# Kernel optimization log

Hardware: AMD Instinct MI355X
Metric: run time of the kernel (lower is better)

The kernel has to match this reference:

```python
import jax, jax.numpy as jnp
import numpy as np

B, T, D_IN, D_OUT, H = 128, 128, 64, 64, 1024


def _lstm_cell(x_t, h, c, W_ih, W_hh, b_ih, b_hh):
    # PyTorch LSTMCell: gates = x@W_ih^T + b_ih + h@W_hh^T + b_hh, order [i, f, g, o]
    g = x_t @ W_ih.T + b_ih + h @ W_hh.T + b_hh  # [B, 4H]
    i, f, gg, o = jnp.split(g, 4, axis=-1)
    c_new = jax.nn.sigmoid(f) * c + jax.nn.sigmoid(i) * jnp.tanh(gg)
    h_new = jax.nn.sigmoid(o) * jnp.tanh(c_new)
    return h_new, c_new


def setup_inputs() -> dict:
    key = jax.random.key(0)
    ks = jax.random.split(key, 16)
    s_in = 1.0 / np.sqrt(H)
    inp = {
        "x": jax.random.normal(ks[0], (B, T, D_IN), dtype=jnp.float32),
        "W_ih1": jax.random.normal(ks[1], (4 * H, D_IN), dtype=jnp.float32) * s_in,
        "W_hh1": jax.random.normal(ks[2], (4 * H, H), dtype=jnp.float32) * s_in,
        "b_ih1": jax.random.normal(ks[3], (4 * H,), dtype=jnp.float32) * s_in,
        "b_hh1": jax.random.normal(ks[4], (4 * H,), dtype=jnp.float32) * s_in,
        "W_ih2": jax.random.normal(ks[5], (4 * H, H), dtype=jnp.float32) * s_in,
        "W_hh2": jax.random.normal(ks[6], (4 * H, H), dtype=jnp.float32) * s_in,
        "b_ih2": jax.random.normal(ks[7], (4 * H,), dtype=jnp.float32) * s_in,
        "b_hh2": jax.random.normal(ks[8], (4 * H,), dtype=jnp.float32) * s_in,
        "W_lin": jax.random.normal(ks[9], (D_IN, H), dtype=jnp.float32) * s_in,
        "b_lin": jax.random.normal(ks[10], (D_IN,), dtype=jnp.float32) * s_in,
        "W_hio": jax.random.normal(ks[11], (D_OUT, H), dtype=jnp.float32) * s_in,
        "b_hio": jax.random.normal(ks[12], (D_OUT,), dtype=jnp.float32) * s_in,
        "future": 1,
    }
    return inp


def reference(x, W_ih1, W_hh1, b_ih1, b_hh1, W_ih2, W_hh2, b_ih2, b_hh2,
              W_lin, b_lin, W_hio, b_hio, future):
    b = x.shape[0]
    h1 = jnp.zeros((b, H), x.dtype)
    c1 = jnp.zeros((b, H), x.dtype)
    h2 = jnp.zeros((b, H), x.dtype)
    c2 = jnp.zeros((b, H), x.dtype)

    def step(carry, x_t):
        h1, c1, h2, c2 = carry
        h1, c1 = _lstm_cell(x_t, h1, c1, W_ih1, W_hh1, b_ih1, b_hh1)
        h2, c2 = _lstm_cell(h1, h2, c2, W_ih2, W_hh2, b_ih2, b_hh2)
        return (h1, c1, h2, c2), None

    (h1, c1, h2, c2), _ = jax.lax.scan(step, (h1, c1, h2, c2),
                                       jnp.swapaxes(x, 0, 1))  # scan over T
    output = h2 @ W_lin.T + b_lin  # [B, D_IN] (only last step's value is used)

    for _ in range(int(future)):
        h1, c1 = _lstm_cell(output, h1, c1, W_ih1, W_hh1, b_ih1, b_hh1)
        h2, c2 = _lstm_cell(h1, h2, c2, W_ih2, W_hh2, b_ih2, b_hh2)
        output = h2 @ W_hio.T + b_hio  # [B, D_OUT]

    return output[:, None, :]  # [B, 1, D_OUT]
```

## Files before the change

kernel.cpp:

```cpp
#include <hip/hip_runtime.h>

#define B_   128
#define T_   128
#define DIN  64
#define H_   1024
#define NBLK 256
#define NTHR 1024

typedef _Float16 f16;
typedef _Float16 half8 __attribute__((ext_vector_type(8)));
typedef float float4v __attribute__((ext_vector_type(4)));
typedef unsigned uint2v __attribute__((ext_vector_type(2)));
typedef unsigned uint4v __attribute__((ext_vector_type(4)));


#define OFF_W2    34816
#define OFF_SG1A  100352
#define OFF_SG1B  109056
#define OFF_SG2A  117760
#define OFF_SG2B  126464
#define OFF_C1    135168
#define OFF_C2    137216
#define OFF_B1    139264
#define OFF_B2    139328
#define SMEM_BYTES 139392


struct Params {
  const float *x, *Wih1, *Whh1, *bih1, *bhh1, *Wih2, *Whh2, *bih2, *bhh2,
              *Wlin, *blin, *Whio, *bhio;
  const int* fut;
  float* out;
  f16 *x16, *h1a, *h1b, *h2a, *h2b, *ob;
  unsigned *arrive, *rel;
  unsigned *S;
};

__device__ __forceinline__ float sigm(float v) { return 1.f / (1.f + __expf(-v)); }
__device__ __forceinline__ float tanh_(float v) { return 2.f / (1.f + __expf(-2.f * v)) - 1.f; }

__device__ __forceinline__ unsigned get_xcc() {
  unsigned x;
  asm volatile("s_getreg_b32 %0, hwreg(HW_REG_XCC_ID)" : "=s"(x));
  return x & 15u;
}

__device__ __forceinline__ void grid_sync(unsigned* arrive, unsigned* rel, unsigned ph) {
  __syncthreads();
  const int tid = threadIdx.x, bid = blockIdx.x;
  if (bid == 0) {
    if (tid > 0 && tid < NBLK) {
      while (__hip_atomic_load(&arrive[tid], __ATOMIC_RELAXED, __HIP_MEMORY_SCOPE_AGENT) != ph)
        __builtin_amdgcn_s_sleep(8);
    }
    __syncthreads();
    if (tid == 0)
      __hip_atomic_store(rel, ph, __ATOMIC_RELEASE, __HIP_MEMORY_SCOPE_AGENT);
  } else {
    if (tid == 0) {
      __hip_atomic_store(&arrive[bid], ph, __ATOMIC_RELEASE, __HIP_MEMORY_SCOPE_AGENT);
      while (__hip_atomic_load(rel, __ATOMIC_RELAXED, __HIP_MEMORY_SCOPE_AGENT) != ph)
        __builtin_amdgcn_s_sleep(8);
    }
  }
  __syncthreads();
  __builtin_amdgcn_fence(__ATOMIC_ACQUIRE, "agent");
}

__device__ __forceinline__ void fast_sync(unsigned* S, unsigned x, unsigned xtotal,
                                          unsigned nxcd, unsigned ph) {
  __syncthreads();
  if (threadIdx.x == 0) {
    unsigned t = __hip_atomic_fetch_add(&S[x * 32], 1u, __ATOMIC_RELAXED, __HIP_MEMORY_SCOPE_AGENT);
    bool leader = (t % xtotal == 0u);
    if ((t + 1u) % xtotal == 0u) {
      unsigned c = __hip_atomic_fetch_add(&S[512], 1u, __ATOMIC_RELAXED, __HIP_MEMORY_SCOPE_AGENT);
      if ((c + 1u) % nxcd == 0u)
        __hip_atomic_store(&S[544], ph, __ATOMIC_RELAXED, __HIP_MEMORY_SCOPE_AGENT);
      asm volatile("buffer_inv sc0 sc1\n\ts_waitcnt vmcnt(0)" ::: "memory");
      __hip_atomic_store(&S[1088 + x * 32], ph, __ATOMIC_RELAXED, __HIP_MEMORY_SCOPE_AGENT);
    }
    if (leader) {
      while (__hip_atomic_load(&S[544], __ATOMIC_RELAXED, __HIP_MEMORY_SCOPE_AGENT) != ph)
        __builtin_amdgcn_s_sleep(1);
      while (__hip_atomic_load(&S[1088 + x * 32], __ATOMIC_RELAXED, __HIP_MEMORY_SCOPE_AGENT) != ph)
        __builtin_amdgcn_s_sleep(1);
      __hip_atomic_store(&S[576 + x * 32], ph, __ATOMIC_RELAXED, __HIP_MEMORY_SCOPE_AGENT);
      asm volatile("buffer_inv sc0\n\ts_waitcnt vmcnt(0)" ::: "memory");
    } else {
      while (__hip_atomic_load(&S[576 + x * 32], __ATOMIC_RELAXED, __HIP_MEMORY_SCOPE_AGENT) != ph)
        __builtin_amdgcn_s_sleep(2);
      asm volatile("buffer_inv sc0\n\ts_waitcnt vmcnt(0)" ::: "memory");
    }
  }
  __syncthreads();
}

__global__ void __launch_bounds__(NTHR, 4) lstm_k(Params p) {
  extern __shared__ char smem[];
  f16*   W1s  = (f16*)(smem);
  f16*   W2s  = (f16*)(smem + OFF_W2);
  float* Sg1A = (float*)(smem + OFF_SG1A);
  float* Sg1B = (float*)(smem + OFF_SG1B);
  float* Sg2A = (float*)(smem + OFF_SG2A);
  float* Sg2B = (float*)(smem + OFF_SG2B);
  float* c1   = (float*)(smem + OFF_C1);
  float* c2   = (float*)(smem + OFF_C2);
  float* bs1  = (float*)(smem + OFF_B1);
  float* bs2  = (float*)(smem + OFF_B2);

  const int tid = threadIdx.x, bid = blockIdx.x;
  const int hb  = bid * 4;
  const int fut = p.fut[0];
  const unsigned xcc = get_xcc();
  unsigned* S = p.S;

  if (bid == 0) {
    for (int i = tid; i < 2048; i += NTHR)
      __hip_atomic_store(&S[i], 0u, __ATOMIC_RELAXED, __HIP_MEMORY_SCOPE_AGENT);
  }

  for (int idx = tid; idx < 34 * 512; idx += NTHR) {
    int c = idx >> 9, r = idx & 511;
    int q = r >> 7, colw = (r >> 3) & 15, j = r & 7;
    int k = c * 32 + q * 8 + j;
    int row = (colw >> 2) * H_ + hb + (colw & 3);
    float v = (k < H_) ? p.Whh1[row * H_ + k] : p.Wih1[row * DIN + (k - H_)];
    W1s[idx] = (f16)v;
  }
  for (int idx = tid; idx < 64 * 512; idx += NTHR) {
    int c = idx >> 9, r = idx & 511;
    int q = r >> 7, colw = (r >> 3) & 15, j = r & 7;
    int k = c * 32 + q * 8 + j;
    int row = (colw >> 2) * H_ + hb + (colw & 3);
    float v = (k < H_) ? p.Wih2[row * H_ + k] : p.Whh2[row * H_ + (k - H_)];
    W2s[idx] = (f16)v;
  }
  if (tid < 16) {
    int row = (tid >> 2) * H_ + hb + (tid & 3);
    bs1[tid] = p.bih1[row] + p.bhh1[row];
    bs2[tid] = p.bih2[row] + p.bhh2[row];
  }
  for (int i = tid; i < 512; i += NTHR) { c1[i] = 0.f; c2[i] = 0.f; }
  for (int i = bid * NTHR + tid; i < B_ * T_ * DIN; i += NBLK * NTHR)
    p.x16[i] = (f16)p.x[i];
  for (int i = bid * NTHR + tid; i < B_ * H_; i += NBLK * NTHR) {
    p.h1a[i] = (f16)0.f; p.h1b[i] = (f16)0.f;
    p.h2a[i] = (f16)0.f; p.h2b[i] = (f16)0.f;
  }

  unsigned ph = 1;
  grid_sync(p.arrive, p.rel, ph);
  if (tid == 0)
    __hip_atomic_fetch_add(&S[1600 + xcc], 1u, __ATOMIC_RELAXED, __HIP_MEMORY_SCOPE_AGENT);
  ++ph;
  grid_sync(p.arrive, p.rel, ph);

  unsigned xtotal = __hip_atomic_load(&S[1600 + xcc], __ATOMIC_RELAXED, __HIP_MEMORY_SCOPE_AGENT);
  unsigned nxcd = 0;
  for (int i = 0; i < 16; ++i)
    nxcd += (__hip_atomic_load(&S[1600 + i], __ATOMIC_RELAXED, __HIP_MEMORY_SCOPE_AGENT) != 0u);

  auto gsync = [&]() { ++ph; fast_sync(S, xcc, xtotal, nxcd, ph); };

  const int lane = tid & 63, wq = tid >> 6;
  const int g  = wq >> 3;
  const int wv = wq & 7;
  const int col = lane & 15, quad = lane >> 4;
  const int m0 = wv * 16 + col;
  const int ko = quad * 8;
  const int jb = g * 16;
  const float b1v = g ? 0.f : bs1[col];
  const float b2v = g ? 0.f : bs2[col];
  const f16* W1f = W1s + lane * 8;
  const f16* W2f = W2s + lane * 8;
  float* S1w = g ? Sg1B : Sg1A;
  float* S2w = g ? Sg2B : Sg2A;
  const int hoff = quad * 1024 + m0 * 4;

  f16 *h1c = p.h1a, *h1n = p.h1b, *h2c = p.h2a, *h2n = p.h2b;

  auto lstm_pw = [&](const float* SgA, const float* SgB, float* cst, f16* hn) {
    int mm = tid >> 2, cc = tid & 3;
    int i0 = mm * 17 + cc;
    float gi = SgA[i0]      + SgB[i0];
    float gf = SgA[i0 + 4]  + SgB[i0 + 4];
    float gg = SgA[i0 + 8]  + SgB[i0 + 8];
    float go = SgA[i0 + 12] + SgB[i0 + 12];
    float cn = sigm(gf) * cst[tid] + sigm(gi) * tanh_(gg);
    cst[tid] = cn;
    f16 hv = (f16)(sigm(go) * tanh_(cn));
    int v = (int)__builtin_bit_cast(unsigned short, hv);
    int base = lane & ~3;
    int v0 = __shfl(v, base, 64),     v1 = __shfl(v, base + 1, 64);
    int v2 = __shfl(v, base + 2, 64), v3 = __shfl(v, base + 3, 64);
    if (cc == 0) {
      unsigned long long pk = (unsigned long long)(unsigned short)v0
        | ((unsigned long long)(unsigned short)v1 << 16)
        | ((unsigned long long)(unsigned short)v2 << 32)
        | ((unsigned long long)(unsigned short)v3 << 48);
      __hip_atomic_store((unsigned long long*)(hn + bid * 512 + mm * 4), pk,
                         __ATOMIC_RELAXED, __HIP_MEMORY_SCOPE_AGENT);
    }
  };

  auto ldwin = [&](const f16* hX, int j) -> half8 {
    const uint2v* q0 = (const uint2v*)(hX + j * 4096 + hoff);
    const uint2v* q1 = (const uint2v*)(hX + j * 4096 + hoff + 512);
    uint2v u0 = *q0, u1 = *q1;
    uint4v u = {u0[0], u0[1], u1[0], u1[1]};
    return __builtin_bit_cast(half8, u);
  };

  auto phase = [&](bool l1, bool l2, const f16* xp, int xstr) {
    float4v a1 = {b1v, b1v, b1v, b1v};
    float4v a2 = {b2v, b2v, b2v, b2v};

    if (l1) {
      half8 ax = *(const half8*)(xp + m0 * xstr + g * 32 + ko);
      a1 = __builtin_amdgcn_mfma_f32_16x16x32_f16(ax, *(const half8*)(W1f + (32 + g) * 512), a1, 0, 0, 0);
    }
    if (l1 && l2) {
      #pragma unroll
      for (int i = 0; i < 16; ++i) {
        int j = jb + i;
        half8 w1 = ldwin(h1c, j);
        half8 w2 = ldwin(h2c, j);
        a1 = __builtin_amdgcn_mfma_f32_16x16x32_f16(w1, *(const half8*)(W1f + j * 512), a1, 0, 0, 0);
        a2 = __builtin_amdgcn_mfma_f32_16x16x32_f16(w1, *(const half8*)(W2f + j * 512), a2, 0, 0, 0);
        a2 = __builtin_amdgcn_mfma_f32_16x16x32_f16(w2, *(const half8*)(W2f + (32 + j) * 512), a2, 0, 0, 0);
      }
    } else if (l1) {
      #pragma unroll
      for (int i = 0; i < 16; ++i) {
        int j = jb + i;
        half8 w1 = ldwin(h1c, j);
        a1 = __builtin_amdgcn_mfma_f32_16x16x32_f16(w1, *(const half8*)(W1f + j * 512), a1, 0, 0, 0);
      }
    } else if (l2) {
      #pragma unroll
      for (int i = 0; i < 16; ++i) {
        int j = jb + i;
        half8 w1 = ldwin(h1c, j);
        half8 w2 = ldwin(h2c, j);
        a2 = __builtin_amdgcn_mfma_f32_16x16x32_f16(w1, *(const half8*)(W2f + j * 512), a2, 0, 0, 0);
        a2 = __builtin_amdgcn_mfma_f32_16x16x32_f16(w2, *(const half8*)(W2f + (32 + j) * 512), a2, 0, 0, 0);
      }
    }

    __syncthreads();
    if (l1) {
      #pragma unroll
      for (int r = 0; r < 4; ++r)
        S1w[(wv * 16 + quad * 4 + r) * 17 + col] = a1[r];
    }
    if (l2) {
      #pragma unroll
      for (int r = 0; r < 4; ++r)
        S2w[(wv * 16 + quad * 4 + r) * 17 + col] = a2[r];
    }
    __syncthreads();
    if (tid < 512) {
      if (l1) lstm_pw(Sg1A, Sg1B, c1, h1n);
      if (l2) lstm_pw(Sg2A, Sg2B, c2, h2n);
    }
  };

  auto out_phase = [&](const float* W, const float* bv, bool wout) {
    if (tid >= 512) return;
    int j = bid & 63, mgp = bid >> 6;
    int rid = tid >> 4, ks = tid & 15;
    int mrow = mgp * 32 + rid;
    const float* wr = W + j * H_ + ks * 64;
    float s = 0.f;
    #pragma unroll
    for (int q = 0; q < 16; ++q) {
      const uint2v* hp = (const uint2v*)(h2c + (ks * 16 + q) * 512 + mrow * 4);
      uint2v u = *hp;
      half8 hv4;
      { uint4v t = {u[0], u[1], 0u, 0u}; hv4 = __builtin_bit_cast(half8, t); }
      s += (float)hv4[0] * wr[q * 4 + 0] + (float)hv4[1] * wr[q * 4 + 1]
         + (float)hv4[2] * wr[q * 4 + 2] + (float)hv4[3] * wr[q * 4 + 3];
    }
    s += __shfl_down(s, 8, 16);
    s += __shfl_down(s, 4, 16);
    s += __shfl_down(s, 2, 16);
    s += __shfl_down(s, 1, 16);
    if (ks == 0) {
      float v = s + bv[j];
      f16 hv = (f16)v;
      __hip_atomic_store((unsigned short*)&p.ob[mrow * 64 + j],
                         __builtin_bit_cast(unsigned short, hv),
                         __ATOMIC_RELAXED, __HIP_MEMORY_SCOPE_AGENT);
      if (wout) p.out[mrow * 64 + j] = v;
    }
  };

  for (int t = -1; t < T_; ++t) {
    bool l1 = (t + 1 < T_), l2 = (t >= 0);
    phase(l1, l2, p.x16 + (t + 1) * DIN, T_ * DIN);
    gsync();
    if (l1) { f16* tm = h1c; h1c = h1n; h1n = tm; }
    if (l2) { f16* tm = h2c; h2c = h2n; h2n = tm; }
  }
  out_phase(p.Wlin, p.blin, fut == 0);
  gsync();
  for (int f = 0; f < fut; ++f) {
    phase(true, false, p.ob, 64);
    gsync();
    { f16* tm = h1c; h1c = h1n; h1n = tm; }
    phase(false, true, p.ob, 64);
    gsync();
    { f16* tm = h2c; h2c = h2n; h2n = tm; }
    out_phase(p.Whio, p.bhio, f == fut - 1);
    gsync();
  }
}

extern "C" void kernel_launch(void* const* d_in, const int* in_sizes, int n_in,
                              void* d_out, int out_size, void* d_ws, size_t ws_size,
                              hipStream_t stream) {
  char* w = (char*)d_ws;
  auto carve = [&](size_t n) { char* r = w; w += (n + 255) & ~(size_t)255; return r; };

  Params p;
  p.x    = (const float*)d_in[0];
  p.Wih1 = (const float*)d_in[1];
  p.Whh1 = (const float*)d_in[2];
  p.bih1 = (const float*)d_in[3];
  p.bhh1 = (const float*)d_in[4];
  p.Wih2 = (const float*)d_in[5];
  p.Whh2 = (const float*)d_in[6];
  p.bih2 = (const float*)d_in[7];
  p.bhh2 = (const float*)d_in[8];
  p.Wlin = (const float*)d_in[9];
  p.blin = (const float*)d_in[10];
  p.Whio = (const float*)d_in[11];
  p.bhio = (const float*)d_in[12];
  p.fut  = (const int*)d_in[13];
  p.out  = (float*)d_out;

  p.x16 = (f16*)carve((size_t)B_ * T_ * DIN * 2);
  p.h1a = (f16*)carve((size_t)B_ * H_ * 2);
  p.h1b = (f16*)carve((size_t)B_ * H_ * 2);
  p.h2a = (f16*)carve((size_t)B_ * H_ * 2);
  p.h2b = (f16*)carve((size_t)B_ * H_ * 2);
  p.ob  = (f16*)carve((size_t)B_ * 64 * 2);
  p.arrive = (unsigned*)carve(NBLK * sizeof(unsigned));
  p.rel    = (unsigned*)carve(256);
  p.S      = (unsigned*)carve(2048 * sizeof(unsigned));

  (void)hipFuncSetAttribute((const void*)lstm_k,
                            hipFuncAttributeMaxDynamicSharedMemorySize, SMEM_BYTES);
  void* args[] = { &p };
  (void)hipLaunchCooperativeKernel((void*)lstm_k, dim3(NBLK), dim3(NTHR),
                                   args, SMEM_BYTES, stream);
}
```

Baseline: 1.897 ms.

## Split hidden-unit pairs across block pairs with split-K partial exchange via global buffers

Each pair of blocks (bid and bid^128) now shares 8 hidden units. Each block computes the half of the K dimension selected by g for both 4-unit groups, then passes the partial sums for its partner's units through a global buffer. A per-block flag with a spin-wait synchronises the two blocks. Within a block, the two wave-groups split K into halves and the layer-1 and layer-2 pointwise updates run on separate thread halves. The goal is to cut the per-block h-window loads, since each block now reads only half of h1/h2, and to spread the pointwise work. The cost is extra global partial-sum traffic and a pairwise handshake every timestep.

After: 1.890 ms. Within noise of the previous version (-0.4%).

```diff
diff --git a/kernel.cpp b/kernel.cpp
--- a/kernel.cpp
+++ b/kernel.cpp
@@ -12,7 +12,6 @@
 typedef float float4v __attribute__((ext_vector_type(4)));
 typedef unsigned uint2v __attribute__((ext_vector_type(2)));
 typedef unsigned uint4v __attribute__((ext_vector_type(4)));
-
 
 #define OFF_W2    34816
 #define OFF_SG1A  100352
@@ -25,7 +24,6 @@
 #define OFF_B2    139328
 #define SMEM_BYTES 139392
 
-
 struct Params {
   const float *x, *Wih1, *Whh1, *bih1, *bhh1, *Wih2, *Whh2, *bih2, *bhh2,
               *Wlin, *blin, *Whio, *bhio;
@@ -34,6 +32,8 @@
   f16 *x16, *h1a, *h1b, *h2a, *h2b, *ob;
   unsigned *arrive, *rel;
   unsigned *S;
+  float* PB;
+  unsigned* FL;
 };
 
 __device__ __forceinline__ float sigm(float v) { return 1.f / (1.f + __expf(-v)); }
@@ -110,7 +110,10 @@
   float* bs2  = (float*)(smem + OFF_B2);
 
   const int tid = threadIdx.x, bid = blockIdx.x;
-  const int hb  = bid * 4;
+  const int c   = bid & 127;
+  const int g   = bid >> 7;
+  const int bidp = bid ^ 128;
+  const int cb  = c * 2 + g;
   const int fut = p.fut[0];
   const unsigned xcc = get_xcc();
   unsigned* S = p.S;
@@ -119,25 +122,31 @@
     for (int i = tid; i < 2048; i += NTHR)
       __hip_atomic_store(&S[i], 0u, __ATOMIC_RELAXED, __HIP_MEMORY_SCOPE_AGENT);
   }
-
-  for (int idx = tid; idx < 34 * 512; idx += NTHR) {
-    int c = idx >> 9, r = idx & 511;
-    int q = r >> 7, colw = (r >> 3) & 15, j = r & 7;
-    int k = c * 32 + q * 8 + j;
-    int row = (colw >> 2) * H_ + hb + (colw & 3);
-    float v = (k < H_) ? p.Whh1[row * H_ + k] : p.Wih1[row * DIN + (k - H_)];
+  for (int i = bid * NTHR + tid; i < 256 * 32; i += NBLK * NTHR)
+    __hip_atomic_store(&p.FL[i], 0u, __ATOMIC_RELAXED, __HIP_MEMORY_SCOPE_AGENT);
+
+  for (int idx = tid; idx < 17 * 2 * 512; idx += NTHR) {
+    int j2 = idx >> 9, r = idx & 511;
+    int j = j2 >> 1, nt = j2 & 1;
+    int lane_ = r >> 3, jj = r & 7;
+    int q = lane_ >> 4, colw = lane_ & 15;
+    int row = (colw >> 2) * H_ + c * 8 + nt * 4 + (colw & 3);
+    float v = (j < 16) ? p.Whh1[row * H_ + g * 512 + j * 32 + q * 8 + jj]
+                       : p.Wih1[row * DIN + g * 32 + q * 8 + jj];
     W1s[idx] = (f16)v;
   }
-  for (int idx = tid; idx < 64 * 512; idx += NTHR) {
-    int c = idx >> 9, r = idx & 511;
-    int q = r >> 7, colw = (r >> 3) & 15, j = r & 7;
-    int k = c * 32 + q * 8 + j;
-    int row = (colw >> 2) * H_ + hb + (colw & 3);
-    float v = (k < H_) ? p.Wih2[row * H_ + k] : p.Whh2[row * H_ + (k - H_)];
+  for (int idx = tid; idx < 32 * 2 * 512; idx += NTHR) {
+    int j2 = idx >> 9, r = idx & 511;
+    int j = j2 >> 1, nt = j2 & 1;
+    int lane_ = r >> 3, jj = r & 7;
+    int q = lane_ >> 4, colw = lane_ & 15;
+    int row = (colw >> 2) * H_ + c * 8 + nt * 4 + (colw & 3);
+    float v = (j < 16) ? p.Wih2[row * H_ + g * 512 + j * 32 + q * 8 + jj]
+                       : p.Whh2[row * H_ + g * 512 + (j - 16) * 32 + q * 8 + jj];
     W2s[idx] = (f16)v;
   }
   if (tid < 16) {
-    int row = (tid >> 2) * H_ + hb + (tid & 3);
+    int row = (tid >> 2) * H_ + c * 8 + g * 4 + (tid & 3);
     bs1[tid] = p.bih1[row] + p.bhh1[row];
     bs2[tid] = p.bih2[row] + p.bhh2[row];
   }
@@ -164,32 +173,40 @@
   auto gsync = [&]() { ++ph; fast_sync(S, xcc, xtotal, nxcd, ph); };
 
   const int lane = tid & 63, wq = tid >> 6;
-  const int g  = wq >> 3;
+  const int s  = wq >> 3;
   const int wv = wq & 7;
   const int col = lane & 15, quad = lane >> 4;
   const int m0 = wv * 16 + col;
   const int ko = quad * 8;
-  const int jb = g * 16;
-  const float b1v = g ? 0.f : bs1[col];
-  const float b2v = g ? 0.f : bs2[col];
   const f16* W1f = W1s + lane * 8;
   const f16* W2f = W2s + lane * 8;
-  float* S1w = g ? Sg1B : Sg1A;
-  float* S2w = g ? Sg2B : Sg2A;
+  float* S1w = s ? Sg1B : Sg1A;
+  float* S2w = s ? Sg2B : Sg2A;
   const int hoff = quad * 1024 + m0 * 4;
 
+  auto PBidx = [](int cg, int dg, int ss, int ll) {
+    return ((((cg * 2 + dg) * 2 + ss) * 2 + ll) * 2048);
+  };
+
   f16 *h1c = p.h1a, *h1n = p.h1b, *h2c = p.h2a, *h2n = p.h2b;
-
-  auto lstm_pw = [&](const float* SgA, const float* SgB, float* cst, f16* hn) {
-    int mm = tid >> 2, cc = tid & 3;
+  unsigned pcnt = 0;
+
+  auto lstm_pw = [&](const float* SgA, const float* SgB, float* Pb0, float* Pb1,
+                     const float* bsX, float* cst, f16* hn) {
+    int idx = tid & 511;
+    int mm = idx >> 2, cc = idx & 3;
     int i0 = mm * 17 + cc;
-    float gi = SgA[i0]      + SgB[i0];
-    float gf = SgA[i0 + 4]  + SgB[i0 + 4];
-    float gg = SgA[i0 + 8]  + SgB[i0 + 8];
-    float go = SgA[i0 + 12] + SgB[i0 + 12];
-    float cn = sigm(gf) * cst[tid] + sigm(gi) * tanh_(gg);
-    cst[tid] = cn;
-    f16 hv = (f16)(sigm(go) * tanh_(cn));
+    int pb = mm * 16 + cc;
+    float gq[4];
+    #pragma unroll
+    for (int q = 0; q < 4; ++q) {
+      float pv0 = __hip_atomic_load(Pb0 + pb + q * 4, __ATOMIC_RELAXED, __HIP_MEMORY_SCOPE_AGENT);
+      float pv1 = __hip_atomic_load(Pb1 + pb + q * 4, __ATOMIC_RELAXED, __HIP_MEMORY_SCOPE_AGENT);
+      gq[q] = SgA[i0 + q * 4] + SgB[i0 + q * 4] + pv0 + pv1 + bsX[q * 4 + cc];
+    }
+    float cn = sigm(gq[1]) * cst[idx] + sigm(gq[0]) * tanh_(gq[2]);
+    cst[idx] = cn;
+    f16 hv = (f16)(sigm(gq[3]) * tanh_(cn));
     int v = (int)__builtin_bit_cast(unsigned short, hv);
     int base = lane & ~3;
     int v0 = __shfl(v, base, 64),     v1 = __shfl(v, base + 1, 64);
@@ -199,7 +216,7 @@
         | ((unsigned long long)(unsigned short)v1 << 16)
         | ((unsigned long long)(unsigned short)v2 << 32)
         | ((unsigned long long)(unsigned short)v3 << 48);
-      __hip_atomic_store((unsigned long long*)(hn + bid * 512 + mm * 4), pk,
+      __hip_atomic_store((unsigned long long*)(hn + cb * 512 + mm * 4), pk,
                          __ATOMIC_RELAXED, __HIP_MEMORY_SCOPE_AGENT);
     }
   };
@@ -213,56 +230,79 @@
   };
 
   auto phase = [&](bool l1, bool l2, const f16* xp, int xstr) {
-    float4v a1 = {b1v, b1v, b1v, b1v};
-    float4v a2 = {b2v, b2v, b2v, b2v};
+    ++pcnt;
+    float4v a1A = {0,0,0,0}, a1B = {0,0,0,0};
+    float4v a2A = {0,0,0,0}, a2B = {0,0,0,0};
+
+    if (l1 && s == 0) {
+      half8 ax = *(const half8*)(xp + m0 * xstr + g * 32 + ko);
+      a1A = __builtin_amdgcn_mfma_f32_16x16x32_f16(ax, *(const half8*)(W1f + 32 * 512), a1A, 0, 0, 0);
+      a1B = __builtin_amdgcn_mfma_f32_16x16x32_f16(ax, *(const half8*)(W1f + 33 * 512), a1B, 0, 0, 0);
+    }
+    #pragma unroll
+    for (int i = 0; i < 8; ++i) {
+      int j = s * 8 + i;
+      int gw = g * 16 + j;
+      half8 w1 = ldwin(h1c, gw);
+      if (l1) {
+        a1A = __builtin_amdgcn_mfma_f32_16x16x32_f16(w1, *(const half8*)(W1f + (j * 2) * 512), a1A, 0, 0, 0);
+        a1B = __builtin_amdgcn_mfma_f32_16x16x32_f16(w1, *(const half8*)(W1f + (j * 2 + 1) * 512), a1B, 0, 0, 0);
+      }
+      if (l2) {
+        half8 w2 = ldwin(h2c, gw);
+        a2A = __builtin_amdgcn_mfma_f32_16x16x32_f16(w1, *(const half8*)(W2f + (j * 2) * 512), a2A, 0, 0, 0);
+        a2B = __builtin_amdgcn_mfma_f32_16x16x32_f16(w1, *(const half8*)(W2f + (j * 2 + 1) * 512), a2B, 0, 0, 0);
+        a2A = __builtin_amdgcn_mfma_f32_16x16x32_f16(w2, *(const half8*)(W2f + ((16 + j) * 2) * 512), a2A, 0, 0, 0);
+        a2B = __builtin_amdgcn_mfma_f32_16x16x32_f16(w2, *(const half8*)(W2f + ((16 + j) * 2 + 1) * 512), a2B, 0, 0, 0);
+      }
+    }
+
+    {
+      int mb = (wv * 16 + quad * 4) * 16 + col;
+      if (l1) {
+        float4v pa = g ? a1A : a1B;
+        float* dst = p.PB + PBidx(c, 1 - g, s, 0) + mb;
+        #pragma unroll
+        for (int r = 0; r < 4; ++r)
+          __hip_atomic_store(dst + r * 16, pa[r], __ATOMIC_RELAXED, __HIP_MEMORY_SCOPE_AGENT);
+      }
+      if (l2) {
+        float4v pa = g ? a2A : a2B;
+        float* dst = p.PB + PBidx(c, 1 - g, s, 1) + mb;
+        #pragma unroll
+        for (int r = 0; r < 4; ++r)
+          __hip_atomic_store(dst + r * 16, pa[r], __ATOMIC_RELAXED, __HIP_MEMORY_SCOPE_AGENT);
+      }
+    }
+    __syncthreads();
+    if (tid == 0)
+      __hip_atomic_store(&p.FL[bid * 32], pcnt, __ATOMIC_RELEASE, __HIP_MEMORY_SCOPE_AGENT);
 
     if (l1) {
-      half8 ax = *(const half8*)(xp + m0 * xstr + g * 32 + ko);
-      a1 = __builtin_amdgcn_mfma_f32_16x16x32_f16(ax, *(const half8*)(W1f + (32 + g) * 512), a1, 0, 0, 0);
-    }
-    if (l1 && l2) {
-      #pragma unroll
-      for (int i = 0; i < 16; ++i) {
-        int j = jb + i;
-        half8 w1 = ldwin(h1c, j);
-        half8 w2 = ldwin(h2c, j);
-        a1 = __builtin_amdgcn_mfma_f32_16x16x32_f16(w1, *(const half8*)(W1f + j * 512), a1, 0, 0, 0);
-        a2 = __builtin_amdgcn_mfma_f32_16x16x32_f16(w1, *(const half8*)(W2f + j * 512), a2, 0, 0, 0);
-        a2 = __builtin_amdgcn_mfma_f32_16x16x32_f16(w2, *(const half8*)(W2f + (32 + j) * 512), a2, 0, 0, 0);
-      }
-    } else if (l1) {
-      #pragma unroll
-      for (int i = 0; i < 16; ++i) {
-        int j = jb + i;
-        half8 w1 = ldwin(h1c, j);
-        a1 = __builtin_amdgcn_mfma_f32_16x16x32_f16(w1, *(const half8*)(W1f + j * 512), a1, 0, 0, 0);
-      }
-    } else if (l2) {
-      #pragma unroll
-      for (int i = 0; i < 16; ++i) {
-        int j = jb + i;
-        half8 w1 = ldwin(h1c, j);
-        half8 w2 = ldwin(h2c, j);
-        a2 = __builtin_amdgcn_mfma_f32_16x16x32_f16(w1, *(const half8*)(W2f + j * 512), a2, 0, 0, 0);
-        a2 = __builtin_amdgcn_mfma_f32_16x16x32_f16(w2, *(const half8*)(W2f + (32 + j) * 512), a2, 0, 0, 0);
-      }
-    }
-
-    __syncthreads();
-    if (l1) {
+      float4v oa = g ? a1B : a1A;
       #pragma unroll
       for (int r = 0; r < 4; ++r)
-        S1w[(wv * 16 + quad * 4 + r) * 17 + col] = a1[r];
+        S1w[(wv * 16 + quad * 4 + r) * 17 + col] = oa[r];
     }
     if (l2) {
+      float4v oa = g ? a2B : a2A;
       #pragma unroll
       for (int r = 0; r < 4; ++r)
-        S2w[(wv * 16 + quad * 4 + r) * 17 + col] = a2[r];
+        S2w[(wv * 16 + quad * 4 + r) * 17 + col] = oa[r];
     }
     __syncthreads();
+
+    while (__hip_atomic_load(&p.FL[bidp * 32], __ATOMIC_RELAXED, __HIP_MEMORY_SCOPE_AGENT) < pcnt)
+      __builtin_amdgcn_s_sleep(1);
+
     if (tid < 512) {
-      if (l1) lstm_pw(Sg1A, Sg1B, c1, h1n);
-      if (l2) lstm_pw(Sg2A, Sg2B, c2, h2n);
+      if (l1) lstm_pw(Sg1A, Sg1B,
+                      p.PB + PBidx(c, g, 0, 0), p.PB + PBidx(c, g, 1, 0),
+                      bs1, c1, h1n);
+    } else {
+      if (l2) lstm_pw(Sg2A, Sg2B,
+                      p.PB + PBidx(c, g, 0, 1), p.PB + PBidx(c, g, 1, 1),
+                      bs2, c2, h2n);
     }
   };
 
@@ -272,22 +312,22 @@
     int rid = tid >> 4, ks = tid & 15;
     int mrow = mgp * 32 + rid;
     const float* wr = W + j * H_ + ks * 64;
-    float s = 0.f;
+    float sacc = 0.f;
     #pragma unroll
     for (int q = 0; q < 16; ++q) {
       const uint2v* hp = (const uint2v*)(h2c + (ks * 16 + q) * 512 + mrow * 4);
       uint2v u = *hp;
       half8 hv4;
       { uint4v t = {u[0], u[1], 0u, 0u}; hv4 = __builtin_bit_cast(half8, t); }
-      s += (float)hv4[0] * wr[q * 4 + 0] + (float)hv4[1] * wr[q * 4 + 1]
-         + (float)hv4[2] * wr[q * 4 + 2] + (float)hv4[3] * wr[q * 4 + 3];
-    }
-    s += __shfl_down(s, 8, 16);
-    s += __shfl_down(s, 4, 16);
-    s += __shfl_down(s, 2, 16);
-    s += __shfl_down(s, 1, 16);
+      sacc += (float)hv4[0] * wr[q * 4 + 0] + (float)hv4[1] * wr[q * 4 + 1]
+            + (float)hv4[2] * wr[q * 4 + 2] + (float)hv4[3] * wr[q * 4 + 3];
+    }
+    sacc += __shfl_down(sacc, 8, 16);
+    sacc += __shfl_down(sacc, 4, 16);
+    sacc += __shfl_down(sacc, 2, 16);
+    sacc += __shfl_down(sacc, 1, 16);
     if (ks == 0) {
-      float v = s + bv[j];
+      float v = sacc + bv[j];
       f16 hv = (f16)v;
       __hip_atomic_store((unsigned short*)&p.ob[mrow * 64 + j],
                          __builtin_bit_cast(unsigned short, hv),
@@ -349,6 +389,8 @@
   p.arrive = (unsigned*)carve(NBLK * sizeof(unsigned));
   p.rel    = (unsigned*)carve(256);
   p.S      = (unsigned*)carve(2048 * sizeof(unsigned));
+  p.PB     = (float*)carve((size_t)128 * 2 * 2 * 2 * 2048 * sizeof(float));
+  p.FL     = (unsigned*)carve((size_t)256 * 32 * sizeof(unsigned));
 
   (void)hipFuncSetAttribute((const void*)lstm_k,
                             hipFuncAttributeMaxDynamicSharedMemorySize, SMEM_BYTES);
```
